# Performance work log

Measured on AMD Instinct MI355X. Metric: run time of the kernel, lower is better.

The kernel has to match this reference:

```python
import jax, jax.numpy as jnp
import numpy as np
from itertools import combinations

NDIM = 256
BATCH = 65536


def setup_inputs() -> dict:
    key = jax.random.key(0)
    k1, k2 = jax.random.split(key)
    pairs = np.array(list(combinations(range(NDIM), 2)), dtype=np.int32)  # [comb(ndim,2), 2]
    return {
        "x": jax.random.normal(k1, (BATCH, NDIM), dtype=jnp.float32),
        "rots": jax.random.normal(k2, (pairs.shape[0],), dtype=jnp.float32),
        "idx_i": jnp.asarray(pairs[:, 0]),
        "idx_j": jnp.asarray(pairs[:, 1]),
    }


def _build_mat(rots, idx_i, idx_j, ndim):
    # Equivalent to mat = R_last @ ... @ R_first @ I, then return mat.T.
    # Each Givens rotation R_(i,j,theta) only mixes rows i and j, so we update
    # two rows per step (O(ndim) work) instead of a dense ndim x ndim matmul.
    # Torch uses cfloat, but all imaginary parts are identically zero, so
    # float32 computes the same math.
    def step(mat, t):
        i, j, theta = t
        c = jnp.cos(theta)
        s = jnp.sin(theta)
        ri = mat[i]
        rj = mat[j]
        mat = mat.at[i].set(c * ri - s * rj)
        mat = mat.at[j].set(s * ri + c * rj)
        return mat, None

    mat0 = jnp.eye(ndim, dtype=rots.dtype)
    mat, _ = jax.lax.scan(step, mat0, (idx_i, idx_j, rots))
    return mat.T  # forward does x @ mat.T


def reference(x, rots, idx_i, idx_j):
    m = _build_mat(rots, idx_i, idx_j, x.shape[-1])  # [ndim, ndim]
    return x @ m
```

## Files before the change

kernel.cpp:

```cpp
#include <hip/hip_runtime.h>
#include <hip/hip_bf16.h>
#include <math.h>

#define NDIM 256
#define NROT 32640
#define NSEG 64
#define SEGLEN 510
#define MATE (NDIM * NDIM)
#define NODEE (2 * MATE)

typedef __bf16 bf16x4_t __attribute__((ext_vector_type(4)));
typedef __bf16 bf16x8_t __attribute__((ext_vector_type(8)));
typedef float f32x4_t __attribute__((ext_vector_type(4)));


#define ROT1(RJ, CS) { float nri_ = fmaf((CS).x, ri, -((CS).y * (RJ))); \
                       (RJ) = fmaf((CS).y, ri, (CS).x * (RJ)); ri = nri_; }

#define LOAD16(P, JB, KK) \
    P##0 = *(const f32x4_t*)&tile[(JB)][t][0]; \
    P##1 = *(const f32x4_t*)&tile[(JB)][t][4]; \
    P##2 = *(const f32x4_t*)&tile[(JB) + 1][t][0]; \
    P##3 = *(const f32x4_t*)&tile[(JB) + 1][t][4]; \
    _Pragma("unroll") \
    for (int u = 0; u < 16; u++) P##c[u] = csl[(KK) + u];

#define COMP16(P, JB) \
    _Pragma("unroll") \
    for (int u = 0; u < 4; u++) ROT1(P##0[u], P##c[u]) \
    _Pragma("unroll") \
    for (int u = 0; u < 4; u++) ROT1(P##1[u], P##c[4 + u]) \
    _Pragma("unroll") \
    for (int u = 0; u < 4; u++) ROT1(P##2[u], P##c[8 + u]) \
    _Pragma("unroll") \
    for (int u = 0; u < 4; u++) ROT1(P##3[u], P##c[12 + u]) \
    *(f32x4_t*)&tile[(JB)][t][0] = P##0; \
    *(f32x4_t*)&tile[(JB)][t][4] = P##1; \
    *(f32x4_t*)&tile[(JB) + 1][t][0] = P##2; \
    *(f32x4_t*)&tile[(JB) + 1][t][4] = P##3;

__global__ __launch_bounds__(64, 1) void k_build(const float* __restrict__ rots,
                                                 __bf16* __restrict__ leaves) {
    __shared__ float tile[32][64][8];
    __shared__ float2 csl[SEGLEN + 16];
    const int t = threadIdx.x;
    const int seg = blockIdx.x >> 2;
    const int cg_ = blockIdx.x & 3;
    const int col = cg_ * 64 + t;
    const int kg0 = seg * SEGLEN;

    for (int u = t; u < SEGLEN; u += 64) {
        float th = rots[kg0 + u];
        float s, c;
        sincosf(th, &s, &c);
        csl[u] = make_float2(c, s);
    }
    for (int u = SEGLEN + t; u < SEGLEN + 16; u += 64) csl[u] = make_float2(1.f, 0.f);

    #pragma unroll
    for (int jb = 0; jb < 32; jb++) {
        f32x4_t z0 = {0.f, 0.f, 0.f, 0.f}, z1 = {0.f, 0.f, 0.f, 0.f};
        if ((col >> 3) == jb) {
            if ((col & 7) < 4) z0[col & 3] = 1.0f;
            else               z1[col & 3] = 1.0f;
        }
        *(f32x4_t*)&tile[jb][t][0] = z0;
        *(f32x4_t*)&tile[jb][t][4] = z1;
    }

    int k = 0;
    int i = 0, cum = 0;
    while (cum + (NDIM - 1 - i) <= kg0) { cum += NDIM - 1 - i; i++; }
    int j = i + 1 + (kg0 - cum);

    float* T = &tile[0][0][0];
    #define TADDR(r) ((((r) >> 3) * 512) + t * 8 + ((r) & 7))

    while (k < SEGLEN) {
        float ri = T[TADDR(i)];
        int rem = min(NDIM - j, SEGLEN - k);

        int npeel = min((8 - (j & 7)) & 7, rem);
        for (int u = 0; u < npeel; u++) {
            float2 cs = csl[k];
            float rj = T[TADDR(j)];
            float nri = fmaf(cs.x, ri, -(cs.y * rj));
            T[TADDR(j)] = fmaf(cs.y, ri, cs.x * rj);
            ri = nri; j++; k++;
        }
        rem -= npeel;

        if (rem >= 16) {
            int jb = j >> 3;
            f32x4_t A0, A1, A2, A3, B0, B1, B2, B3;
            float2 Ac[16], Bc[16];
            LOAD16(A, jb, k)
            while (rem >= 48) {
                LOAD16(B, jb + 2, k + 16)
                COMP16(A, jb)
                jb += 2; j += 16; k += 16; rem -= 16;
                LOAD16(A, jb + 2, k + 16)
                COMP16(B, jb)
                jb += 2; j += 16; k += 16; rem -= 16;
            }
            if (rem >= 32) {
                LOAD16(B, jb + 2, k + 16)
                COMP16(A, jb)
                jb += 2; j += 16; k += 16; rem -= 16;
                COMP16(B, jb)
                jb += 2; j += 16; k += 16; rem -= 16;
            } else {
                COMP16(A, jb)
                jb += 2; j += 16; k += 16; rem -= 16;
            }
        }

        if (rem >= 8) {
            int jb = j >> 3;
            f32x4_t a0 = *(const f32x4_t*)&tile[jb][t][0];
            f32x4_t a1 = *(const f32x4_t*)&tile[jb][t][4];
            float2 cc[8];
            #pragma unroll
            for (int u = 0; u < 8; u++) cc[u] = csl[k + u];
            #pragma unroll
            for (int u = 0; u < 4; u++) ROT1(a0[u], cc[u])
            #pragma unroll
            for (int u = 0; u < 4; u++) ROT1(a1[u], cc[4 + u])
            *(f32x4_t*)&tile[jb][t][0] = a0;
            *(f32x4_t*)&tile[jb][t][4] = a1;
            j += 8; k += 8; rem -= 8;
        }

        while (rem > 0) {
            float2 cs = csl[k];
            float rj = T[TADDR(j)];
            float nri = fmaf(cs.x, ri, -(cs.y * rj));
            T[TADDR(j)] = fmaf(cs.y, ri, cs.x * rj);
            ri = nri; j++; k++; rem--;
        }

        T[TADDR(i)] = ri;
        if (j == NDIM) { i++; j = i + 1; }
    }
    #undef TADDR

    __bf16* hi = leaves + (size_t)seg * NODEE;
    __bf16* lo = hi + MATE;
    if (seg & 1) {
        for (int jb = 0; jb < 32; jb++) {
            f32x4_t v0 = *(const f32x4_t*)&tile[jb][t][0];
            f32x4_t v1 = *(const f32x4_t*)&tile[jb][t][4];
            #pragma unroll
            for (int u = 0; u < 8; u++) {
                float v = (u < 4) ? v0[u & 3] : v1[u & 3];
                __bf16 h = (__bf16)v;
                hi[(size_t)(jb * 8 + u) * NDIM + col] = h;
                lo[(size_t)(jb * 8 + u) * NDIM + col] = (__bf16)(v - (float)h);
            }
        }
    } else {
        for (int jb = 0; jb < 32; jb++) {
            f32x4_t v0 = *(const f32x4_t*)&tile[jb][t][0];
            f32x4_t v1 = *(const f32x4_t*)&tile[jb][t][4];
            bf16x8_t vh, vl;
            #pragma unroll
            for (int u = 0; u < 8; u++) {
                float v = (u < 4) ? v0[u & 3] : v1[u & 3];
                __bf16 h = (__bf16)v;
                vh[u] = h;
                vl[u] = (__bf16)(v - (float)h);
            }
            *(bf16x8_t*)&hi[(size_t)col * NDIM + jb * 8] = vh;
            *(bf16x8_t*)&lo[(size_t)col * NDIM + jb * 8] = vl;
        }
    }
}

#define LDK 264
__global__ __launch_bounds__(256) void k_combine(const __bf16* __restrict__ src,
                                                 __bf16* __restrict__ dst,
                                                 int finalLevel) {
    __shared__ __bf16 planes[4][64 * LDK];

    const int p = blockIdx.x >> 4;
    const int qd = blockIdx.x & 15;
    const int rbq = (qd >> 2) * 64;
    const int cbq = (qd & 3) * 64;
    const __bf16* A = src + (size_t)(2 * p) * NODEE;
    const __bf16* B = src + (size_t)(2 * p + 1) * NODEE;
    __bf16* Chi = dst + (size_t)p * NODEE;
    __bf16* Clo = Chi + MATE;
    const bool storeT = (!finalLevel) && ((p & 1) == 0);

    const int t = threadIdx.x;
    const int wid = t >> 6, lane = t & 63;
    const int wr2 = (wid >> 1) * 32, wc2 = (wid & 1) * 32;
    const int lrow = lane & 15, kg = lane >> 4;

    const __bf16* plane_src[4] = {B, B + MATE, A, A + MATE};
    const int plane_row0[4] = {rbq, rbq, cbq, cbq};
    #pragma unroll
    for (int q = 0; q < 32; q++) {
        int g = q * 256 + t;
        int pl = g >> 11;
        int c = g & 2047;
        int row = c >> 5, sg = c & 31;
        bf16x8_t v = *(const bf16x8_t*)&plane_src[pl][(size_t)(plane_row0[pl] + row) * NDIM + sg * 8];
        *(bf16x8_t*)&planes[pl][row * LDK + sg * 8] = v;
    }
    __syncthreads();

    f32x4_t acc[2][2] = {};
    #pragma unroll
    for (int kc = 0; kc < 8; kc++) {
        bf16x8_t afh[2], afl[2], bfh[2], bfl[2];
        #pragma unroll
        for (int mt = 0; mt < 2; mt++) {
            int r = (wr2 + mt * 16 + lrow) * LDK + kc * 32 + kg * 8;
            afh[mt] = *(const bf16x8_t*)&planes[0][r];
            afl[mt] = *(const bf16x8_t*)&planes[1][r];
        }
        #pragma unroll
        for (int nt = 0; nt < 2; nt++) {
            int r = (wc2 + nt * 16 + lrow) * LDK + kc * 32 + kg * 8;
            bfh[nt] = *(const bf16x8_t*)&planes[2][r];
            bfl[nt] = *(const bf16x8_t*)&planes[3][r];
        }
        #pragma unroll
        for (int mt = 0; mt < 2; mt++)
            #pragma unroll
            for (int nt = 0; nt < 2; nt++) {
                acc[mt][nt] = __builtin_amdgcn_mfma_f32_16x16x32_bf16(afh[mt], bfh[nt], acc[mt][nt], 0, 0, 0);
                acc[mt][nt] = __builtin_amdgcn_mfma_f32_16x16x32_bf16(afh[mt], bfl[nt], acc[mt][nt], 0, 0, 0);
                acc[mt][nt] = __builtin_amdgcn_mfma_f32_16x16x32_bf16(afl[mt], bfh[nt], acc[mt][nt], 0, 0, 0);
            }
    }

    #pragma unroll
    for (int mt = 0; mt < 2; mt++)
        #pragma unroll
        for (int nt = 0; nt < 2; nt++) {
            int grow = rbq + wr2 + mt * 16 + kg * 4;
            int gcol = cbq + wc2 + nt * 16 + lrow;
            if (storeT) {
                bf16x4_t vh, vl;
                #pragma unroll
                for (int r = 0; r < 4; r++) {
                    float v = acc[mt][nt][r];
                    __bf16 h = (__bf16)v;
                    vh[r] = h;
                    vl[r] = (__bf16)(v - (float)h);
                }
                *(bf16x4_t*)&Chi[(size_t)gcol * NDIM + grow] = vh;
                *(bf16x4_t*)&Clo[(size_t)gcol * NDIM + grow] = vl;
            } else if (finalLevel) {
                #pragma unroll
                for (int r = 0; r < 4; r++)
                    Chi[(size_t)(grow + r) * NDIM + gcol] = (__bf16)acc[mt][nt][r];
            } else {
                #pragma unroll
                for (int r = 0; r < 4; r++) {
                    float v = acc[mt][nt][r];
                    __bf16 h = (__bf16)v;
                    Chi[(size_t)(grow + r) * NDIM + gcol] = h;
                    Clo[(size_t)(grow + r) * NDIM + gcol] = (__bf16)(v - (float)h);
                }
            }
        }
}

#define LDM 264
__global__ __launch_bounds__(512, 1) void k_gemm(const float* __restrict__ X,
                                                 const __bf16* __restrict__ Mhi,
                                                 float* __restrict__ Y) {
    __shared__ __bf16 Ms[128 * LDM];
    const int bx = blockIdx.x;
    const int rg = bx & 255;
    const int ch = bx >> 8;
    const int t = threadIdx.x;
    const int wid = t >> 6, lane = t & 63;
    const int lrow = lane & 15, kg = lane >> 4;

    #pragma unroll
    for (int q = 0; q < 8; q++) {
        int g = q * 512 + t;
        int row = g >> 5, sg = g & 31;
        bf16x8_t v = *(const bf16x8_t*)&Mhi[(size_t)(ch * 128 + row) * 256 + sg * 8];
        *(bf16x8_t*)&Ms[row * LDM + sg * 8] = v;
    }
    __syncthreads();

    const int row0 = rg * 256 + wid * 32;
    #pragma unroll
    for (int sl = 0; sl < 2; sl++) {
        const int rb = row0 + sl * 16;
        f32x4_t acc[8] = {};
        #pragma unroll
        for (int kc = 0; kc < 8; kc++) {
            const float* xp = &X[(size_t)(rb + lrow) * 256 + kc * 32 + kg * 8];
            f32x4_t x0 = *(const f32x4_t*)xp;
            f32x4_t x1 = *(const f32x4_t*)(xp + 4);
            bf16x8_t af;
            af[0] = (__bf16)x0.x; af[1] = (__bf16)x0.y;
            af[2] = (__bf16)x0.z; af[3] = (__bf16)x0.w;
            af[4] = (__bf16)x1.x; af[5] = (__bf16)x1.y;
            af[6] = (__bf16)x1.z; af[7] = (__bf16)x1.w;
            #pragma unroll
            for (int nt = 0; nt < 8; nt++) {
                bf16x8_t bf = *(const bf16x8_t*)&Ms[(nt * 16 + lrow) * LDM + kc * 32 + kg * 8];
                acc[nt] = __builtin_amdgcn_mfma_f32_16x16x32_bf16(af, bf, acc[nt], 0, 0, 0);
            }
        }
        #pragma unroll
        for (int nt = 0; nt < 8; nt++)
            #pragma unroll
            for (int r = 0; r < 4; r++)
                Y[(size_t)(rb + kg * 4 + r) * 256 + ch * 128 + nt * 16 + lrow] = acc[nt][r];
    }
}

extern "C" void kernel_launch(void* const* d_in, const int* in_sizes, int n_in,
                              void* d_out, int out_size, void* d_ws, size_t ws_size,
                              hipStream_t stream) {
    const float* x = (const float*)d_in[0];
    const float* rots = (const float*)d_in[1];
    float* out = (float*)d_out;

    __bf16* B0 = (__bf16*)d_ws;
    __bf16* B1 = B0 + (size_t)NSEG * NODEE;

    k_build<<<NSEG * 4, 64, 0, stream>>>(rots, B0);
    k_combine<<<32 * 16, 256, 0, stream>>>(B0, B1, 0);
    k_combine<<<16 * 16, 256, 0, stream>>>(B1, B0, 0);
    k_combine<<<8 * 16, 256, 0, stream>>>(B0, B1, 0);
    k_combine<<<4 * 16, 256, 0, stream>>>(B1, B0, 0);
    k_combine<<<2 * 16, 256, 0, stream>>>(B0, B1, 0);
    k_combine<<<1 * 16, 256, 0, stream>>>(B1, B0, 1);
    k_gemm<<<512, 512, 0, stream>>>(x, B0, out);
}
```

Baseline: 223.5 us.

## Balance build segments on row boundaries and prefetch X before GEMM sync

The build kernel now splits the rotation sequence into segments that end on whole rows, sized by a cost model (fixed per-row cost plus per-rotation cost). This removes the mid-row start/stop logic and aims to even out work across blocks, whose per-row peel overhead varied. Separately, the GEMM kernel issues all global loads of its X rows into registers before the shared-memory barrier, so that load latency overlaps the weight staging. The price is higher register pressure, and variable segment lengths need a larger shared cs buffer.

```diff
diff --git a/kernel.cpp b/kernel.cpp
--- a/kernel.cpp
+++ b/kernel.cpp
@@ -5,9 +5,12 @@
 #define NDIM 256
 #define NROT 32640
 #define NSEG 64
-#define SEGLEN 510
 #define MATE (NDIM * NDIM)
 #define NODEE (2 * MATE)
+
+#define BF 1280
+#define BC 16
+#define CSLMAX 1104
 
 typedef __bf16 bf16x4_t __attribute__((ext_vector_type(4)));
 typedef __bf16 bf16x8_t __attribute__((ext_vector_type(8)));
@@ -39,23 +42,45 @@
     *(f32x4_t*)&tile[(JB) + 1][t][0] = P##2; \
     *(f32x4_t*)&tile[(JB) + 1][t][4] = P##3;
 
+__device__ __forceinline__ int run_off(int r) {
+    return 255 * r - (r * (r - 1)) / 2;
+}
+__device__ __forceinline__ int cum_cost(int r) {
+    return BF * r + BC * run_off(r);
+}
+__device__ __forceinline__ int seg_boundary(int s) {
+    if (s <= 0) return 0;
+    if (s >= NSEG) return 255;
+    const long target = ((long)cum_cost(255) * s) / NSEG;
+    int lo = 0, hi = 255;
+    while (lo < hi) {
+        int mid = (lo + hi) >> 1;
+        if ((long)cum_cost(mid) >= target) hi = mid; else lo = mid + 1;
+    }
+    return lo;
+}
+
 __global__ __launch_bounds__(64, 1) void k_build(const float* __restrict__ rots,
                                                  __bf16* __restrict__ leaves) {
     __shared__ float tile[32][64][8];
-    __shared__ float2 csl[SEGLEN + 16];
+    __shared__ float2 csl[CSLMAX];
     const int t = threadIdx.x;
     const int seg = blockIdx.x >> 2;
     const int cg_ = blockIdx.x & 3;
     const int col = cg_ * 64 + t;
-    const int kg0 = seg * SEGLEN;
-
-    for (int u = t; u < SEGLEN; u += 64) {
+
+    const int r0 = seg_boundary(seg);
+    const int r1 = seg_boundary(seg + 1);
+    const int kg0 = run_off(r0);
+    const int nrot = run_off(r1) - kg0;
+
+    for (int u = t; u < nrot; u += 64) {
         float th = rots[kg0 + u];
         float s, c;
         sincosf(th, &s, &c);
         csl[u] = make_float2(c, s);
     }
-    for (int u = SEGLEN + t; u < SEGLEN + 16; u += 64) csl[u] = make_float2(1.f, 0.f);
+    for (int u = nrot + t; u < nrot + 16 && u < CSLMAX; u += 64) csl[u] = make_float2(1.f, 0.f);
 
     #pragma unroll
     for (int jb = 0; jb < 32; jb++) {
@@ -68,17 +93,14 @@
         *(f32x4_t*)&tile[jb][t][4] = z1;
     }
 
-    int k = 0;
-    int i = 0, cum = 0;
-    while (cum + (NDIM - 1 - i) <= kg0) { cum += NDIM - 1 - i; i++; }
-    int j = i + 1 + (kg0 - cum);
-
     float* T = &tile[0][0][0];
     #define TADDR(r) ((((r) >> 3) * 512) + t * 8 + ((r) & 7))
 
-    while (k < SEGLEN) {
+    int k = 0;
+    for (int i = r0; i < r1; ++i) {
         float ri = T[TADDR(i)];
-        int rem = min(NDIM - j, SEGLEN - k);
+        int j = i + 1;
+        int rem = NDIM - j;
 
         int npeel = min((8 - (j & 7)) & 7, rem);
         for (int u = 0; u < npeel; u++) {
@@ -140,7 +162,6 @@
         }
 
         T[TADDR(i)] = ri;
-        if (j == NDIM) { i++; j = i + 1; }
     }
     #undef TADDR
 
@@ -288,23 +309,34 @@
         bf16x8_t v = *(const bf16x8_t*)&Mhi[(size_t)(ch * 128 + row) * 256 + sg * 8];
         *(bf16x8_t*)&Ms[row * LDM + sg * 8] = v;
     }
+
+    const int row0 = rg * 256 + wid * 32;
+    const float* xb0 = &X[(size_t)(row0 + lrow) * 256 + kg * 8];
+    const float* xb1 = xb0 + 16 * 256;
+
+    f32x4_t xa[16], xbq[16];
+    #pragma unroll
+    for (int kc = 0; kc < 8; kc++) {
+        xa[2 * kc]     = *(const f32x4_t*)(xb0 + kc * 32);
+        xa[2 * kc + 1] = *(const f32x4_t*)(xb0 + kc * 32 + 4);
+    }
+    #pragma unroll
+    for (int kc = 0; kc < 8; kc++) {
+        xbq[2 * kc]     = *(const f32x4_t*)(xb1 + kc * 32);
+        xbq[2 * kc + 1] = *(const f32x4_t*)(xb1 + kc * 32 + 4);
+    }
     __syncthreads();
 
-    const int row0 = rg * 256 + wid * 32;
-    #pragma unroll
-    for (int sl = 0; sl < 2; sl++) {
-        const int rb = row0 + sl * 16;
+    {
         f32x4_t acc[8] = {};
         #pragma unroll
         for (int kc = 0; kc < 8; kc++) {
-            const float* xp = &X[(size_t)(rb + lrow) * 256 + kc * 32 + kg * 8];
-            f32x4_t x0 = *(const f32x4_t*)xp;
-            f32x4_t x1 = *(const f32x4_t*)(xp + 4);
             bf16x8_t af;
-            af[0] = (__bf16)x0.x; af[1] = (__bf16)x0.y;
-            af[2] = (__bf16)x0.z; af[3] = (__bf16)x0.w;
-            af[4] = (__bf16)x1.x; af[5] = (__bf16)x1.y;
-            af[6] = (__bf16)x1.z; af[7] = (__bf16)x1.w;
+            #pragma unroll
+            for (int u = 0; u < 4; u++) {
+                af[u]     = (__bf16)xa[2 * kc][u];
+                af[4 + u] = (__bf16)xa[2 * kc + 1][u];
+            }
             #pragma unroll
             for (int nt = 0; nt < 8; nt++) {
                 bf16x8_t bf = *(const bf16x8_t*)&Ms[(nt * 16 + lrow) * LDM + kc * 32 + kg * 8];
@@ -315,7 +347,29 @@
         for (int nt = 0; nt < 8; nt++)
             #pragma unroll
             for (int r = 0; r < 4; r++)
-                Y[(size_t)(rb + kg * 4 + r) * 256 + ch * 128 + nt * 16 + lrow] = acc[nt][r];
+                Y[(size_t)(row0 + kg * 4 + r) * 256 + ch * 128 + nt * 16 + lrow] = acc[nt][r];
+    }
+    {
+        f32x4_t acc[8] = {};
+        #pragma unroll
+        for (int kc = 0; kc < 8; kc++) {
+            bf16x8_t af;
+            #pragma unroll
+            for (int u = 0; u < 4; u++) {
+                af[u]     = (__bf16)xbq[2 * kc][u];
+                af[4 + u] = (__bf16)xbq[2 * kc + 1][u];
+            }
+            #pragma unroll
+            for (int nt = 0; nt < 8; nt++) {
+                bf16x8_t bf = *(const bf16x8_t*)&Ms[(nt * 16 + lrow) * LDM + kc * 32 + kg * 8];
+                acc[nt] = __builtin_amdgcn_mfma_f32_16x16x32_bf16(af, bf, acc[nt], 0, 0, 0);
+            }
+        }
+        #pragma unroll
+        for (int nt = 0; nt < 8; nt++)
+            #pragma unroll
+            for (int r = 0; r < 4; r++)
+                Y[(size_t)(row0 + 16 + kg * 4 + r) * 256 + ch * 128 + nt * 16 + lrow] = acc[nt][r];
     }
 }
 
```

After: 218.8 us. 2.1% less time.

## Align build segments to row boundaries and widen GEMM tile to full output

Applied to the files above, without the earlier changes.

The build kernel now splits rotations into segments that end on whole rows i, using a cost model (fixed plus per-rotation) and a binary search for balanced boundaries. This removes the mid-row start and end handling and the peeling that partial rows need. Segment sizes now vary, so the cos/sin buffer is sized to a worst-case maximum. Separately, the GEMM now has each block hold the whole 256x256 bf16 matrix in LDS and compute all 256 output columns. X is read and converted once rather than twice, at the cost of half as many blocks, more accumulators and a larger shared allocation.

```diff
diff --git a/kernel.cpp b/kernel.cpp
--- a/kernel.cpp
+++ b/kernel.cpp
@@ -5,9 +5,12 @@
 #define NDIM 256
 #define NROT 32640
 #define NSEG 64
-#define SEGLEN 510
 #define MATE (NDIM * NDIM)
 #define NODEE (2 * MATE)
+
+#define BF 1280
+#define BC 16
+#define CSLMAX 1104
 
 typedef __bf16 bf16x4_t __attribute__((ext_vector_type(4)));
 typedef __bf16 bf16x8_t __attribute__((ext_vector_type(8)));
@@ -39,23 +42,45 @@
     *(f32x4_t*)&tile[(JB) + 1][t][0] = P##2; \
     *(f32x4_t*)&tile[(JB) + 1][t][4] = P##3;
 
+__device__ __forceinline__ int run_off(int r) {
+    return 255 * r - (r * (r - 1)) / 2;
+}
+__device__ __forceinline__ int cum_cost(int r) {
+    return BF * r + BC * run_off(r);
+}
+__device__ __forceinline__ int seg_boundary(int s) {
+    if (s <= 0) return 0;
+    if (s >= NSEG) return 255;
+    const long target = ((long)cum_cost(255) * s) / NSEG;
+    int lo = 0, hi = 255;
+    while (lo < hi) {
+        int mid = (lo + hi) >> 1;
+        if ((long)cum_cost(mid) >= target) hi = mid; else lo = mid + 1;
+    }
+    return lo;
+}
+
 __global__ __launch_bounds__(64, 1) void k_build(const float* __restrict__ rots,
                                                  __bf16* __restrict__ leaves) {
     __shared__ float tile[32][64][8];
-    __shared__ float2 csl[SEGLEN + 16];
+    __shared__ float2 csl[CSLMAX];
     const int t = threadIdx.x;
     const int seg = blockIdx.x >> 2;
     const int cg_ = blockIdx.x & 3;
     const int col = cg_ * 64 + t;
-    const int kg0 = seg * SEGLEN;
-
-    for (int u = t; u < SEGLEN; u += 64) {
+
+    const int r0 = seg_boundary(seg);
+    const int r1 = seg_boundary(seg + 1);
+    const int kg0 = run_off(r0);
+    const int nrot = run_off(r1) - kg0;
+
+    for (int u = t; u < nrot; u += 64) {
         float th = rots[kg0 + u];
         float s, c;
         sincosf(th, &s, &c);
         csl[u] = make_float2(c, s);
     }
-    for (int u = SEGLEN + t; u < SEGLEN + 16; u += 64) csl[u] = make_float2(1.f, 0.f);
+    for (int u = nrot + t; u < nrot + 16 && u < CSLMAX; u += 64) csl[u] = make_float2(1.f, 0.f);
 
     #pragma unroll
     for (int jb = 0; jb < 32; jb++) {
@@ -68,17 +93,14 @@
         *(f32x4_t*)&tile[jb][t][4] = z1;
     }
 
-    int k = 0;
-    int i = 0, cum = 0;
-    while (cum + (NDIM - 1 - i) <= kg0) { cum += NDIM - 1 - i; i++; }
-    int j = i + 1 + (kg0 - cum);
-
     float* T = &tile[0][0][0];
     #define TADDR(r) ((((r) >> 3) * 512) + t * 8 + ((r) & 7))
 
-    while (k < SEGLEN) {
+    int k = 0;
+    for (int i = r0; i < r1; ++i) {
         float ri = T[TADDR(i)];
-        int rem = min(NDIM - j, SEGLEN - k);
+        int j = i + 1;
+        int rem = NDIM - j;
 
         int npeel = min((8 - (j & 7)) & 7, rem);
         for (int u = 0; u < npeel; u++) {
@@ -140,7 +162,6 @@
         }
 
         T[TADDR(i)] = ri;
-        if (j == NDIM) { i++; j = i + 1; }
     }
     #undef TADDR
 
@@ -273,28 +294,26 @@
 __global__ __launch_bounds__(512, 1) void k_gemm(const float* __restrict__ X,
                                                  const __bf16* __restrict__ Mhi,
                                                  float* __restrict__ Y) {
-    __shared__ __bf16 Ms[128 * LDM];
-    const int bx = blockIdx.x;
-    const int rg = bx & 255;
-    const int ch = bx >> 8;
+    __shared__ __bf16 Ms[256 * LDM];
+    const int rg = blockIdx.x;
     const int t = threadIdx.x;
     const int wid = t >> 6, lane = t & 63;
     const int lrow = lane & 15, kg = lane >> 4;
 
     #pragma unroll
-    for (int q = 0; q < 8; q++) {
+    for (int q = 0; q < 16; q++) {
         int g = q * 512 + t;
         int row = g >> 5, sg = g & 31;
-        bf16x8_t v = *(const bf16x8_t*)&Mhi[(size_t)(ch * 128 + row) * 256 + sg * 8];
+        bf16x8_t v = *(const bf16x8_t*)&Mhi[(size_t)row * 256 + sg * 8];
         *(bf16x8_t*)&Ms[row * LDM + sg * 8] = v;
     }
     __syncthreads();
 
     const int row0 = rg * 256 + wid * 32;
-    #pragma unroll
+    #pragma unroll 1
     for (int sl = 0; sl < 2; sl++) {
         const int rb = row0 + sl * 16;
-        f32x4_t acc[8] = {};
+        f32x4_t acc[16] = {};
         #pragma unroll
         for (int kc = 0; kc < 8; kc++) {
             const float* xp = &X[(size_t)(rb + lrow) * 256 + kc * 32 + kg * 8];
@@ -306,16 +325,16 @@
             af[4] = (__bf16)x1.x; af[5] = (__bf16)x1.y;
             af[6] = (__bf16)x1.z; af[7] = (__bf16)x1.w;
             #pragma unroll
-            for (int nt = 0; nt < 8; nt++) {
+            for (int nt = 0; nt < 16; nt++) {
                 bf16x8_t bf = *(const bf16x8_t*)&Ms[(nt * 16 + lrow) * LDM + kc * 32 + kg * 8];
                 acc[nt] = __builtin_amdgcn_mfma_f32_16x16x32_bf16(af, bf, acc[nt], 0, 0, 0);
             }
         }
         #pragma unroll
-        for (int nt = 0; nt < 8; nt++)
+        for (int nt = 0; nt < 16; nt++)
             #pragma unroll
             for (int r = 0; r < 4; r++)
-                Y[(size_t)(rb + kg * 4 + r) * 256 + ch * 128 + nt * 16 + lrow] = acc[nt][r];
+                Y[(size_t)(rb + kg * 4 + r) * 256 + nt * 16 + lrow] = acc[nt][r];
     }
 }
 
@@ -336,5 +355,5 @@
     k_combine<<<4 * 16, 256, 0, stream>>>(B1, B0, 0);
     k_combine<<<2 * 16, 256, 0, stream>>>(B0, B1, 0);
     k_combine<<<1 * 16, 256, 0, stream>>>(B1, B0, 1);
-    k_gemm<<<512, 512, 0, stream>>>(x, B0, out);
-}
+    k_gemm<<<256, 512, 0, stream>>>(x, B0, out);
+}
```

Result: slower. 355.8 us (+59.2%).
